# Performance work log

Measured on AMD Instinct MI355X. Metric: run time of the kernel, lower is better.

Reference implementation:

```python
import jax, jax.numpy as jnp
import numpy as np

D = 4096          # in = out features of the quantized linear
K = 128           # n_quantize (codebook size)
B, S = 4, 4096    # batch, seq_len


def setup_inputs() -> dict:
    key = jax.random.key(0)
    k1, k2, k3, k4 = jax.random.split(key, 4)
    x = jax.random.normal(k1, (B, S, D), dtype=jnp.float32)
    quantized_vectors = jax.random.normal(k2, (D, K), dtype=jnp.float32)
    assignments = jax.random.randint(k3, (D,), 0, K, dtype=jnp.int32)
    bias = jax.random.normal(k4, (D,), dtype=jnp.float32)
    return {"x": x, "quantized_vectors": quantized_vectors,
            "assignments": assignments, "bias": bias}


def reference(x, quantized_vectors, assignments, bias):
    orig_shape = x.shape
    x_flat = x.reshape(-1, quantized_vectors.shape[0])          # [T, D]
    # row-gather the codebook then skinny matmul: [T, D] @ [D, K] -> [T, K]
    gathered = jnp.take(quantized_vectors, assignments, axis=0)  # [D, K]
    qm = jnp.einsum('ij,jk->ik', x_flat, gathered)               # [T, K]
    # column gather back to D outputs, add bias
    out = jnp.take(qm, assignments, axis=1) + bias[None, :]      # [T, D]
    return out.reshape(orig_shape)
```

## Files before the change

### kernel.cpp

```cpp
#include <hip/hip_runtime.h>

#define DD 4096
#define KK 128
#define MAXHC 48

__global__ void vq_build(const int* __restrict__ assign,
                         unsigned short* __restrict__ perm2,
                         int* __restrict__ maxh) {
    __shared__ int cnt[KK];
    __shared__ int off[KK];
    const int tid = threadIdx.x;

    if (tid < KK) cnt[tid] = 0;
    for (int i = tid; i < MAXHC * 256; i += 256)
        perm2[i] = (unsigned short)DD;
    __syncthreads();

    for (int j = tid; j < DD; j += 256)
        atomicAdd(&cnt[assign[j]], 1);
    __syncthreads();

    if (tid == 0) {
        int m = 0;
        for (int c = 0; c < KK; ++c) {
            off[c] = 0;
            int h = (cnt[c] + 1) >> 1;
            if (h > m) m = h;
        }
        *maxh = (m < MAXHC) ? m : MAXHC;
    }
    __syncthreads();

    for (int j = tid; j < DD; j += 256) {
        const int c = assign[j];
        const int p = atomicAdd(&off[c], 1);
        const int i = p >> 1;
        const int th = 2 * c + (p & 1);
        if (i < MAXHC)
            perm2[(i >> 1) * 512 + th * 2 + (i & 1)] = (unsigned short)j;
    }
}

__global__ __launch_bounds__(256) void vq_main(
    const float* __restrict__ x,
    const float* __restrict__ qv,
    const int*   __restrict__ assign,
    const float* __restrict__ bias,
    const unsigned int* __restrict__ pu,
    const int* __restrict__ maxh,
    float* __restrict__ out)
{
    __shared__ float xl[DD + 4];
    __shared__ float xs[KK];
    __shared__ float qm[KK];

    const int t   = blockIdx.x;
    const int tid = threadIdx.x;

    const float4* xrow = reinterpret_cast<const float4*>(x + (size_t)t * DD);
    float4* xl4 = reinterpret_cast<float4*>(xl);
    #pragma unroll
    for (int i = 0; i < 4; ++i)
        xl4[tid + i * 256] = xrow[tid + i * 256];
    if (tid == 0) xl[DD] = 0.0f;
    __syncthreads();

    {
        const int mh2 = (*maxh + 1) >> 1;
        float acc = 0.0f;
        for (int ii = 0; ii < mh2; ++ii) {
            const unsigned int pp = pu[ii * 256 + tid];
            acc += xl[pp & 0xFFFFu];
            acc += xl[pp >> 16];
        }
        acc += __shfl_xor(acc, 1);
        if ((tid & 1) == 0) xs[tid >> 1] = acc;
    }
    __syncthreads();

    {
        const int k    = tid & (KK - 1);
        const int half = tid >> 7;
        float acc = 0.0f;
        const int c0 = half * 64;
        #pragma unroll 8
        for (int c = c0; c < c0 + 64; ++c)
            acc += xs[c] * qv[c * KK + k];
        if (half == 0) qm[k] = acc;
        __syncthreads();
        if (half == 1) qm[k] += acc;
        __syncthreads();
    }

    const int4*   a4   = reinterpret_cast<const int4*>(assign);
    const float4* b4   = reinterpret_cast<const float4*>(bias);
    float4*       out4 = reinterpret_cast<float4*>(out + (size_t)t * DD);
    #pragma unroll
    for (int i = 0; i < 4; ++i) {
        const int idx = tid + i * 256;
        const int4   a = a4[idx];
        const float4 b = b4[idx];
        float4 r;
        r.x = qm[a.x] + b.x;
        r.y = qm[a.y] + b.y;
        r.z = qm[a.z] + b.z;
        r.w = qm[a.w] + b.w;
        out4[idx] = r;
    }
}

extern "C" void kernel_launch(void* const* d_in, const int* in_sizes, int n_in,
                              void* d_out, int out_size, void* d_ws, size_t ws_size,
                              hipStream_t stream) {
    const float* x      = (const float*)d_in[0];
    const float* qv     = (const float*)d_in[1];
    const int*   assign = (const int*)d_in[2];
    const float* bias   = (const float*)d_in[3];
    float*       out    = (float*)d_out;

    unsigned short* perm2 = (unsigned short*)d_ws;
    int* maxh = (int*)((char*)d_ws + MAXHC * 256 * sizeof(unsigned short));

    const int T = in_sizes[0] / DD;

    vq_build<<<dim3(1), dim3(256), 0, stream>>>(assign, perm2, maxh);
    vq_main<<<dim3(T), dim3(256), 0, stream>>>(
        x, qv, assign, bias, (const unsigned int*)perm2, maxh, out);
}
```

Before: 465.4 us.

## Process two token rows per block and pre-interleave codebook into float4 layout

Each block now handles two tokens, so the permutation index loads, assign/bias loads and codebook reads are shared across both rows. A second block in the build kernel repacks the codebook so each thread reads float4 groups of four codebook rows. The small matmul then needs no split-half reduction or extra syncs. The cost is double the LDS footprint per block and half as many blocks, which may lower occupancy. It also assumes T is even.

```diff
diff --git a/kernel.cpp b/kernel.cpp
--- a/kernel.cpp
+++ b/kernel.cpp
@@ -3,13 +3,32 @@
 #define DD 4096
 #define KK 128
 #define MAXHC 48
+#define XROW 4100
+#define QVC_OFF 24832
 
-__global__ void vq_build(const int* __restrict__ assign,
+__global__ void vq_build(const float* __restrict__ qv,
+                         const int* __restrict__ assign,
                          unsigned short* __restrict__ perm2,
-                         int* __restrict__ maxh) {
+                         int* __restrict__ maxh,
+                         float4* __restrict__ qvC) {
+    const int tid = threadIdx.x;
+
+    if (blockIdx.x == 1) {
+        for (int idx = tid; idx < 4096; idx += 256) {
+            const int c4 = idx >> 7;
+            const int k  = idx & (KK - 1);
+            float4 v;
+            v.x = qv[(4 * c4 + 0) * KK + k];
+            v.y = qv[(4 * c4 + 1) * KK + k];
+            v.z = qv[(4 * c4 + 2) * KK + k];
+            v.w = qv[(4 * c4 + 3) * KK + k];
+            qvC[idx] = v;
+        }
+        return;
+    }
+
     __shared__ int cnt[KK];
     __shared__ int off[KK];
-    const int tid = threadIdx.x;
 
     if (tid < KK) cnt[tid] = 0;
     for (int i = tid; i < MAXHC * 256; i += 256)
@@ -43,69 +62,92 @@
 
 __global__ __launch_bounds__(256) void vq_main(
     const float* __restrict__ x,
-    const float* __restrict__ qv,
     const int*   __restrict__ assign,
     const float* __restrict__ bias,
     const unsigned int* __restrict__ pu,
     const int* __restrict__ maxh,
+    const float4* __restrict__ qvC,
     float* __restrict__ out)
 {
-    __shared__ float xl[DD + 4];
-    __shared__ float xs[KK];
-    __shared__ float qm[KK];
+    __shared__ float xl[2 * XROW];
+    __shared__ float xs[2 * KK];
+    __shared__ float qm2[2 * KK];
 
-    const int t   = blockIdx.x;
+    const int t0  = blockIdx.x * 2;
     const int tid = threadIdx.x;
 
-    const float4* xrow = reinterpret_cast<const float4*>(x + (size_t)t * DD);
-    float4* xl4 = reinterpret_cast<float4*>(xl);
+    const float4* r0 = reinterpret_cast<const float4*>(x + (size_t)t0 * DD);
+    const float4* r1 = reinterpret_cast<const float4*>(x + (size_t)(t0 + 1) * DD);
+    float4* xl40 = reinterpret_cast<float4*>(xl);
+    float4* xl41 = reinterpret_cast<float4*>(xl + XROW);
     #pragma unroll
-    for (int i = 0; i < 4; ++i)
-        xl4[tid + i * 256] = xrow[tid + i * 256];
-    if (tid == 0) xl[DD] = 0.0f;
+    for (int i = 0; i < 4; ++i) {
+        xl40[tid + i * 256] = r0[tid + i * 256];
+        xl41[tid + i * 256] = r1[tid + i * 256];
+    }
+    if (tid == 0) { xl[DD] = 0.0f; xl[XROW + DD] = 0.0f; }
     __syncthreads();
 
     {
         const int mh2 = (*maxh + 1) >> 1;
-        float acc = 0.0f;
+        float a0 = 0.0f, a1 = 0.0f;
         for (int ii = 0; ii < mh2; ++ii) {
             const unsigned int pp = pu[ii * 256 + tid];
-            acc += xl[pp & 0xFFFFu];
-            acc += xl[pp >> 16];
+            const int i0 = pp & 0xFFFFu;
+            const int i1 = pp >> 16;
+            a0 += xl[i0];
+            a0 += xl[i1];
+            a1 += xl[XROW + i0];
+            a1 += xl[XROW + i1];
         }
-        acc += __shfl_xor(acc, 1);
-        if ((tid & 1) == 0) xs[tid >> 1] = acc;
+        a0 += __shfl_xor(a0, 1);
+        a1 += __shfl_xor(a1, 1);
+        if ((tid & 1) == 0) {
+            xs[tid >> 1]      = a0;
+            xs[KK + (tid >> 1)] = a1;
+        }
     }
     __syncthreads();
 
     {
-        const int k    = tid & (KK - 1);
-        const int half = tid >> 7;
-        float acc = 0.0f;
-        const int c0 = half * 64;
+        const int k  = tid & (KK - 1);
+        const int tt = tid >> 7;
+        const float4* xs4 = reinterpret_cast<const float4*>(xs + tt * KK);
+        float ax = 0.f, ay = 0.f, az = 0.f, aw = 0.f;
         #pragma unroll 8
-        for (int c = c0; c < c0 + 64; ++c)
-            acc += xs[c] * qv[c * KK + k];
-        if (half == 0) qm[k] = acc;
-        __syncthreads();
-        if (half == 1) qm[k] += acc;
-        __syncthreads();
+        for (int c4 = 0; c4 < 32; ++c4) {
+            const float4 q = qvC[c4 * KK + k];
+            const float4 v = xs4[c4];
+            ax += q.x * v.x;
+            ay += q.y * v.y;
+            az += q.z * v.z;
+            aw += q.w * v.w;
+        }
+        qm2[2 * k + tt] = (ax + ay) + (az + aw);
     }
+    __syncthreads();
 
     const int4*   a4   = reinterpret_cast<const int4*>(assign);
     const float4* b4   = reinterpret_cast<const float4*>(bias);
-    float4*       out4 = reinterpret_cast<float4*>(out + (size_t)t * DD);
+    const float2* qmf2 = reinterpret_cast<const float2*>(qm2);
+    float4* o0 = reinterpret_cast<float4*>(out + (size_t)t0 * DD);
+    float4* o1 = reinterpret_cast<float4*>(out + (size_t)(t0 + 1) * DD);
     #pragma unroll
     for (int i = 0; i < 4; ++i) {
         const int idx = tid + i * 256;
         const int4   a = a4[idx];
         const float4 b = b4[idx];
-        float4 r;
-        r.x = qm[a.x] + b.x;
-        r.y = qm[a.y] + b.y;
-        r.z = qm[a.z] + b.z;
-        r.w = qm[a.w] + b.w;
-        out4[idx] = r;
+        const float2 qx = qmf2[a.x];
+        const float2 qy = qmf2[a.y];
+        const float2 qz = qmf2[a.z];
+        const float2 qw = qmf2[a.w];
+        float4 s0, s1;
+        s0.x = qx.x + b.x;  s1.x = qx.y + b.x;
+        s0.y = qy.x + b.y;  s1.y = qy.y + b.y;
+        s0.z = qz.x + b.z;  s1.z = qz.y + b.z;
+        s0.w = qw.x + b.w;  s1.w = qw.y + b.w;
+        o0[idx] = s0;
+        o1[idx] = s1;
     }
 }
 
@@ -119,11 +161,12 @@
     float*       out    = (float*)d_out;
 
     unsigned short* perm2 = (unsigned short*)d_ws;
-    int* maxh = (int*)((char*)d_ws + MAXHC * 256 * sizeof(unsigned short));
+    int*    maxh = (int*)((char*)d_ws + MAXHC * 256 * sizeof(unsigned short));
+    float4* qvC  = (float4*)((char*)d_ws + QVC_OFF);
 
     const int T = in_sizes[0] / DD;
 
-    vq_build<<<dim3(1), dim3(256), 0, stream>>>(assign, perm2, maxh);
-    vq_main<<<dim3(T), dim3(256), 0, stream>>>(
-        x, qv, assign, bias, (const unsigned int*)perm2, maxh, out);
+    vq_build<<<dim3(2), dim3(256), 0, stream>>>(qv, assign, perm2, maxh, qvC);
+    vq_main<<<dim3(T / 2), dim3(256), 0, stream>>>(
+        x, assign, bias, (const unsigned int*)perm2, maxh, qvC, out);
 }
```

New measurement: 458.5 us. Within noise of the previous version (-1.5%).
